# Kernel tuning notes

Hardware: AMD Instinct MI355X
Metric: run time of the kernel (lower is better)

The kernel has to match this reference:

```python
import jax, jax.numpy as jnp
import numpy as np

H = 200
W = 200
SH = 2.0  # h / h_meters = 200/100
SW = 2.0
THRESH = 0.05   # opacity prune threshold
CHUNK = 128     # gaussians per scan step
EPS_T = 1e-4    # 3DGS transmittance early-stop
ALPHA_MIN = 1.0 / 255.0


def _rasterize(means3D, colors, opac, cov3D):
    """Orthographic BEV 3D-Gaussian-splat rasterization for one sample.
    means3D (N,3), colors (N,d), opac (N,1), cov3D (N,6) packed [xx,xy,xz,yy,yz,zz].
    Returns (d, H, W) image. Depth is identically 0 under the BEV view matrix,
    so compositing order is the input order (stable), matching the CUDA sort.
    """
    N, d = colors.shape
    P = H * W
    # pixel centers, row-major flatten: p = y*W + x
    gy, gx = jnp.meshgrid(jnp.arange(H, dtype=jnp.float32),
                          jnp.arange(W, dtype=jnp.float32), indexing='ij')
    pxf = gx.reshape(-1)
    pyf = gy.reshape(-1)

    # project means with full_proj_transform: u = -sh*y + H/2, v = -sw*x + W/2
    u = -SH * means3D[:, 1] + H / 2.0
    v = -SW * means3D[:, 0] + W / 2.0

    # 2D covariance: W2 @ Cov3D @ W2^T + 0.3*I with W2 = [[0,sh,0],[sw,0,0]]
    a = SH * SH * cov3D[:, 3] + 0.3   # var along image x (from Sigma_yy)
    c = SW * SW * cov3D[:, 0] + 0.3   # var along image y (from Sigma_xx)
    b = SH * SW * cov3D[:, 1]
    det = a * c - b * b
    valid = det > 0.0
    det_s = jnp.where(valid, det, 1.0)
    conA = c / det_s
    conB = b / det_s   # power uses +conB*dx*dy (conic.y = -b/det in CUDA)
    conC = a / det_s

    # fold pruning mask (opacity threshold) and validity into opacity
    op = jnp.where((opac[:, 0] > THRESH) & valid, opac[:, 0], 0.0)

    K = N // CHUNK
    chunks = tuple(t.reshape(K, CHUNK, *t.shape[1:])
                   for t in (u, v, conA, conB, conC, op, colors))

    def body(carry, ch):
        img, T = carry  # img (P,d), T (P,)
        u_, v_, A_, B_, C_, op_, col_ = ch
        dx = u_[:, None] - pxf[None, :]          # (C,P)
        dy = v_[:, None] - pyf[None, :]
        power = -0.5 * (A_[:, None] * dx * dx + C_[:, None] * dy * dy) \
                + B_[:, None] * dx * dy
        alpha = jnp.minimum(0.99, op_[:, None] * jnp.exp(jnp.minimum(power, 0.0)))
        # CUDA skips power>0 and alpha < 1/255
        alpha = jnp.where((power > 0.0) | (alpha < ALPHA_MIN), 0.0, alpha)
        # early termination: skip gaussian i (and all after) once T would drop < 1e-4
        T_incl = T[None, :] * jnp.cumprod(1.0 - alpha, axis=0)
        alpha = jnp.where(T_incl < EPS_T, 0.0, alpha)
        cp = jnp.cumprod(1.0 - alpha, axis=0)    # inclusive products
        T_excl = jnp.concatenate([jnp.ones((1, P), dtype=cp.dtype), cp[:-1]], axis=0)
        wgt = alpha * T_excl * T[None, :]        # (C,P)
        img = img + jnp.einsum('cp,cd->pd', wgt, col_)
        T = T * cp[-1]
        return (img, T), None

    img0 = jnp.zeros((P, d), dtype=colors.dtype)
    T0 = jnp.ones((P,), dtype=colors.dtype)
    (img, T), _ = jax.lax.scan(body, (img0, T0), chunks)
    # background is zeros -> no bg term; reshape to (d, H, W)
    return img.reshape(H, W, d).transpose(2, 0, 1)


def setup_inputs() -> dict:
    key = jax.random.key(0)
    k1, k2, k3, k4 = jax.random.split(key, 4)
    B, N, D = 2, 1024, 32
    features = jax.random.normal(k1, (B, N, D), dtype=jnp.float32)
    # BEV covers +/-50m; scale positions so most gaussians land on the canvas
    means3D = jax.random.normal(k2, (B, N, 3), dtype=jnp.float32) * 20.0
    cov3D = jax.random.uniform(k3, (B, N, 6), dtype=jnp.float32)
    opacities = jax.random.uniform(k4, (B, N, 1), dtype=jnp.float32)
    return {"features": features, "means3D": means3D,
            "cov3D": cov3D, "opacities": opacities}


def reference(features, means3D, cov3D, opacities):
    bev = jax.vmap(_rasterize)(means3D, features, opacities, cov3D)  # (B,d,H,W)
    mask = opacities[..., 0] > THRESH
    mean_count = mask.astype(jnp.float32).sum(axis=1).mean()
    return bev, mean_count
```

## Files before the change

### kernel.cpp

```cpp
#include <hip/hip_runtime.h>


#define HH 200
#define WW 200
#define DD 32
#define NG 1024
#define BB 2
#define OUT_IMG (BB*DD*HH*WW)
#define NW 4
#define SEGG (NG/NW)
#define NGRP (SEGG/64)

__global__ __launch_bounds__(64*NW) void render_kernel(
    const float* __restrict__ feats,
    const float* __restrict__ means,
    const float* __restrict__ cov,
    const float* __restrict__ opac,
    float* __restrict__ out)
{
    __shared__ float su[NW][64], sv[NW][64], sA[NW][64], sB[NW][64],
                     sC[NW][64], sop[NW][64], spl[NW][64];
    __shared__ int   sg[NW][64];
    __shared__ float4 simg[NW][64][8];
    __shared__ float sT[NW][64];
    __shared__ float wsum[NW];

    const int b    = blockIdx.z;
    const int tid  = threadIdx.x;
    const int lane = tid & 63;
    const int wid  = tid >> 6;
    const int px   = blockIdx.x*8 + (lane & 7);
    const int py   = blockIdx.y*8 + (lane >> 3);
    const float pxf = (float)px, pyf = (float)py;
    const float cx  = blockIdx.x*8 + 3.5f;
    const float cy  = blockIdx.y*8 + 3.5f;

    const float* __restrict__ featsB = feats + (size_t)b * NG * DD;
    const int gB = b * NG;

    float4 acc[8];
#pragma unroll
    for (int j = 0; j < 8; ++j) acc[j] = make_float4(0.f,0.f,0.f,0.f);
    float T = 1.f, P = 1.f;
    bool skip = false;

    for (int k = 0; k < NGRP; ++k) {
        const int gl = wid*SEGG + k*64 + lane;
        const int g  = gB + gl;
        const float o  = opac[g];
        const float c0 = cov[g*6+0], c1 = cov[g*6+1], c3 = cov[g*6+3];
        const float av = 4.f*c3 + 0.3f;
        const float cv = 4.f*c0 + 0.3f;
        const float bv = 4.f*c1;
        const float det = av*cv - bv*bv;
        bool flag = false;
        float u=0.f, v=0.f, A=0.f, Bc=0.f, Cc=0.f, pl=0.f;
        if (o > 0.05f && det > 0.f) {
            const float inv = 1.f/det;
            A = cv*inv; Bc = bv*inv; Cc = av*inv;
            u = -2.f*means[g*3+1] + 100.f;
            v = -2.f*means[g*3+0] + 100.f;
            pl = -__logf(255.f*o);
            const float qmax = -2.f*pl;
            const float htr = 0.5f*(A+Cc), hdf = 0.5f*(A-Cc);
            const float lmin = htr - sqrtf(hdf*hdf + Bc*Bc);
            const float r = sqrtf(qmax/lmin) + 0.5f;
            flag = (fabsf(u - cx) <= 3.5f + r) && (fabsf(v - cy) <= 3.5f + r);
        }
        const unsigned long long mask = __ballot(flag);
        const int m = (int)__popcll(mask);
        __syncthreads();
        if (flag) {
            const int pos = (int)__popcll(mask & ((1ull << lane) - 1ull));
            su[wid][pos]=u;  sv[wid][pos]=v;  sA[wid][pos]=A;  sB[wid][pos]=Bc;
            sC[wid][pos]=Cc; sop[wid][pos]=o; spl[wid][pos]=pl; sg[wid][pos]=gl;
        }
        __syncthreads();

        if (!skip) {
            for (int i = 0; i < m; ++i) {
                const float dx = su[wid][i] - pxf;
                const float dy = sv[wid][i] - pyf;
                const float pw = fmaf(sB[wid][i], dx*dy,
                                      -0.5f*(sA[wid][i]*dx*dx + sC[wid][i]*dy*dy));
                if (pw > 0.f) continue;
                if (pw < spl[wid][i] - 1e-3f) continue;
                const float alpha = fminf(0.99f, sop[wid][i] * __expf(pw));
                if (alpha < (1.f/255.f)) continue;
                const float om = 1.f - alpha;
                const float tp = T * P;
                if (tp * om < 1e-4f) { skip = true; break; }
                const float w = alpha * tp;
                const float4* __restrict__ col =
                    (const float4*)(featsB + (size_t)sg[wid][i] * DD);
#pragma unroll
                for (int j = 0; j < 8; ++j) {
                    const float4 c4 = col[j];
                    acc[j].x = fmaf(w, c4.x, acc[j].x);
                    acc[j].y = fmaf(w, c4.y, acc[j].y);
                    acc[j].z = fmaf(w, c4.z, acc[j].z);
                    acc[j].w = fmaf(w, c4.w, acc[j].w);
                }
                P *= om;
            }
        }
        if (k & 1) { T *= P; P = 1.f; skip = false; }
    }

    sT[wid][lane] = T;
#pragma unroll
    for (int j = 0; j < 8; ++j)
        simg[wid][lane][(j + lane) & 7] = acc[j];
    __syncthreads();

    {
        const int p   = tid & 63;
        const int grp = tid >> 6;
        const float t0 = sT[0][p], t1 = sT[1][p], t2 = sT[2][p];
        const float pf1 = t0, pf2 = t0*t1, pf3 = pf2*t2;
        const int ppx = blockIdx.x*8 + (p & 7);
        const int ppy = blockIdx.y*8 + (p >> 3);
        const size_t base = (size_t)b * DD * (HH*WW) + (size_t)ppy * WW + ppx;
#pragma unroll
        for (int q = 0; q < 2; ++q) {
            const int c4 = grp*2 + q;
            const int slot = (c4 + p) & 7;
            const float4 r0 = simg[0][p][slot];
            const float4 r1 = simg[1][p][slot];
            const float4 r2 = simg[2][p][slot];
            const float4 r3 = simg[3][p][slot];
            float4 ov;
            ov.x = fmaf(pf3, r3.x, fmaf(pf2, r2.x, fmaf(pf1, r1.x, r0.x)));
            ov.y = fmaf(pf3, r3.y, fmaf(pf2, r2.y, fmaf(pf1, r1.y, r0.y)));
            ov.z = fmaf(pf3, r3.z, fmaf(pf2, r2.z, fmaf(pf1, r1.z, r0.z)));
            ov.w = fmaf(pf3, r3.w, fmaf(pf2, r2.w, fmaf(pf1, r1.w, r0.w)));
            out[base + (size_t)(c4*4+0)*(HH*WW)] = ov.x;
            out[base + (size_t)(c4*4+1)*(HH*WW)] = ov.y;
            out[base + (size_t)(c4*4+2)*(HH*WW)] = ov.z;
            out[base + (size_t)(c4*4+3)*(HH*WW)] = ov.w;
        }
    }

    if (blockIdx.x == 0 && blockIdx.y == 0 && b == 0) {
        float s = 0.f;
        for (int i = tid; i < BB*NG; i += 64*NW)
            s += (opac[i] > 0.05f) ? 1.f : 0.f;
#pragma unroll
        for (int off = 32; off > 0; off >>= 1)
            s += __shfl_down(s, off, 64);
        if (lane == 0) wsum[wid] = s;
        __syncthreads();
        if (tid == 0)
            out[OUT_IMG] = (wsum[0]+wsum[1]+wsum[2]+wsum[3]) * (1.f/(float)BB);
    }
}

extern "C" void kernel_launch(void* const* d_in, const int* in_sizes, int n_in,
                              void* d_out, int out_size, void* d_ws, size_t ws_size,
                              hipStream_t stream) {
    const float* feats = (const float*)d_in[0];
    const float* means = (const float*)d_in[1];
    const float* cvr   = (const float*)d_in[2];
    const float* opc   = (const float*)d_in[3];
    float* out = (float*)d_out;

    render_kernel<<<dim3(WW/8, HH/8, BB), dim3(64*NW), 0, stream>>>(
        feats, means, cvr, opc, out);
}
```

Measured before the change: 77.59 us.

## Broadcast gaussian params via readlane instead of LDS compaction with block barriers

Replaces the per-group shared-memory compaction, and the two __syncthreads around it, with a ballot mask walked by ctz. Each surviving gaussian's parameters are broadcast from its owning lane with readlane, so waves no longer wait on each other every group. It also computes the culling radius from the covariance eigenvalue directly, does the reciprocal only for survivors, vectorises the covariance load and adds an occupancy hint to launch bounds. Risks include readlane with a lane index that may not be uniform, and a slightly different cull radius that could change which gaussians are kept.

```diff
diff --git a/kernel.cpp b/kernel.cpp
--- a/kernel.cpp
+++ b/kernel.cpp
@@ -11,16 +11,17 @@
 #define SEGG (NG/NW)
 #define NGRP (SEGG/64)
 
-__global__ __launch_bounds__(64*NW) void render_kernel(
+__device__ __forceinline__ float rlane(float x, int l) {
+    return __uint_as_float(__builtin_amdgcn_readlane(__float_as_uint(x), l));
+}
+
+__global__ __launch_bounds__(64*NW, 4) void render_kernel(
     const float* __restrict__ feats,
     const float* __restrict__ means,
     const float* __restrict__ cov,
     const float* __restrict__ opac,
     float* __restrict__ out)
 {
-    __shared__ float su[NW][64], sv[NW][64], sA[NW][64], sB[NW][64],
-                     sC[NW][64], sop[NW][64], spl[NW][64];
-    __shared__ int   sg[NW][64];
     __shared__ float4 simg[NW][64][8];
     __shared__ float sT[NW][64];
     __shared__ float wsum[NW];
@@ -45,54 +46,56 @@
     bool skip = false;
 
     for (int k = 0; k < NGRP; ++k) {
-        const int gl = wid*SEGG + k*64 + lane;
-        const int g  = gB + gl;
-        const float o  = opac[g];
-        const float c0 = cov[g*6+0], c1 = cov[g*6+1], c3 = cov[g*6+3];
-        const float av = 4.f*c3 + 0.3f;
-        const float cv = 4.f*c0 + 0.3f;
-        const float bv = 4.f*c1;
+        const int gbase = wid*SEGG + k*64;
+        const int g  = gB + gbase + lane;
+        const float o   = opac[g];
+        const float2 c01 = *(const float2*)(cov + (size_t)g*6);
+        const float c3  = cov[(size_t)g*6 + 3];
+        const float av = 4.f*c3    + 0.3f;
+        const float cv = 4.f*c01.x + 0.3f;
+        const float bv = 4.f*c01.y;
         const float det = av*cv - bv*bv;
         bool flag = false;
         float u=0.f, v=0.f, A=0.f, Bc=0.f, Cc=0.f, pl=0.f;
         if (o > 0.05f && det > 0.f) {
-            const float inv = 1.f/det;
-            A = cv*inv; Bc = bv*inv; Cc = av*inv;
-            u = -2.f*means[g*3+1] + 100.f;
-            v = -2.f*means[g*3+0] + 100.f;
+            u = -2.f*means[(size_t)g*3+1] + 100.f;
+            v = -2.f*means[(size_t)g*3+0] + 100.f;
             pl = -__logf(255.f*o);
             const float qmax = -2.f*pl;
-            const float htr = 0.5f*(A+Cc), hdf = 0.5f*(A-Cc);
-            const float lmin = htr - sqrtf(hdf*hdf + Bc*Bc);
-            const float r = sqrtf(qmax/lmin) + 0.5f;
-            flag = (fabsf(u - cx) <= 3.5f + r) && (fabsf(v - cy) <= 3.5f + r);
+            const float htr = 0.5f*(av+cv), hdf = 0.5f*(av-cv);
+            const float lmax = htr + sqrtf(hdf*hdf + bv*bv);
+            const float r = sqrtf(qmax*lmax) + 0.5f;
+            if (fabsf(u - cx) <= 3.5f + r && fabsf(v - cy) <= 3.5f + r) {
+                const float inv = 1.f/det;
+                A = cv*inv; Bc = bv*inv; Cc = av*inv;
+                flag = true;
+            }
         }
-        const unsigned long long mask = __ballot(flag);
-        const int m = (int)__popcll(mask);
-        __syncthreads();
-        if (flag) {
-            const int pos = (int)__popcll(mask & ((1ull << lane) - 1ull));
-            su[wid][pos]=u;  sv[wid][pos]=v;  sA[wid][pos]=A;  sB[wid][pos]=Bc;
-            sC[wid][pos]=Cc; sop[wid][pos]=o; spl[wid][pos]=pl; sg[wid][pos]=gl;
-        }
-        __syncthreads();
-
+        unsigned long long mm = __ballot(flag);
         if (!skip) {
-            for (int i = 0; i < m; ++i) {
-                const float dx = su[wid][i] - pxf;
-                const float dy = sv[wid][i] - pyf;
-                const float pw = fmaf(sB[wid][i], dx*dy,
-                                      -0.5f*(sA[wid][i]*dx*dx + sC[wid][i]*dy*dy));
+            while (mm) {
+                const int i = (int)__builtin_ctzll(mm);
+                mm &= mm - 1ull;
+                const float ui  = rlane(u,  i);
+                const float vi  = rlane(v,  i);
+                const float Ai  = rlane(A,  i);
+                const float Bi  = rlane(Bc, i);
+                const float Ci  = rlane(Cc, i);
+                const float oi  = rlane(o,  i);
+                const float pli = rlane(pl, i);
+                const float dx = ui - pxf;
+                const float dy = vi - pyf;
+                const float pw = fmaf(Bi, dx*dy, -0.5f*(Ai*dx*dx + Ci*dy*dy));
                 if (pw > 0.f) continue;
-                if (pw < spl[wid][i] - 1e-3f) continue;
-                const float alpha = fminf(0.99f, sop[wid][i] * __expf(pw));
+                if (pw < pli - 1e-3f) continue;
+                const float alpha = fminf(0.99f, oi * __expf(pw));
                 if (alpha < (1.f/255.f)) continue;
                 const float om = 1.f - alpha;
                 const float tp = T * P;
                 if (tp * om < 1e-4f) { skip = true; break; }
                 const float w = alpha * tp;
                 const float4* __restrict__ col =
-                    (const float4*)(featsB + (size_t)sg[wid][i] * DD);
+                    (const float4*)(featsB + (size_t)(gbase + i) * DD);
 #pragma unroll
                 for (int j = 0; j < 8; ++j) {
                     const float4 c4 = col[j];
@@ -107,7 +110,7 @@
         if (k & 1) { T *= P; P = 1.f; skip = false; }
     }
 
-    sT[wid][lane] = T;
+    sT[wid][lane] = T * P;
 #pragma unroll
     for (int j = 0; j < 8; ++j)
         simg[wid][lane][(j + lane) & 7] = acc[j];
```

After: 72.76 us. -6.2%, faster.
